# Kernel tuning notes

Measured on AMD Instinct MI355X. Metric: run time of the kernel, lower is better.

The kernel has to match this reference:

```python
import jax, jax.numpy as jnp
import numpy as np

H = 32        # num query heads
KVH = 8       # num kv heads
HD = 64       # head dim
G = H // KVH  # GQA group size
THETA = 10000.0


def _rope(x, pos):
    # x: [B, h, S, HD], pos: [B, S] int
    inv_freq = 1.0 / (THETA ** (jnp.arange(0, HD, 2, dtype=jnp.float32) / HD))  # [HD/2]
    freqs = pos.astype(jnp.float32)[:, :, None] * inv_freq[None, None, :]        # [B, S, HD/2]
    emb = jnp.concatenate([freqs, freqs], axis=-1)                               # [B, S, HD]
    cos = jnp.cos(emb)[:, None, :, :].astype(x.dtype)                            # [B, 1, S, HD]
    sin = jnp.sin(emb)[:, None, :, :].astype(x.dtype)
    x1, x2 = x[..., : HD // 2], x[..., HD // 2 :]
    rot = jnp.concatenate([-x2, x1], axis=-1)
    return x * cos + rot * sin


def setup_inputs() -> dict:
    key = jax.random.key(0)
    ks = jax.random.split(key, 8)
    B, S, D = 2, 2048, 2048
    s = 0.02
    hidden_states = jax.random.normal(ks[0], (B, S, D), dtype=jnp.float32)
    position_ids = jnp.broadcast_to(jnp.arange(S, dtype=jnp.int32)[None, :], (B, S))
    Wq = jax.random.normal(ks[1], (H * HD, D), dtype=jnp.float32) * s
    bq = jax.random.normal(ks[2], (H * HD,), dtype=jnp.float32) * s
    Wk = jax.random.normal(ks[3], (KVH * HD, D), dtype=jnp.float32) * s
    bk = jax.random.normal(ks[4], (KVH * HD,), dtype=jnp.float32) * s
    Wv = jax.random.normal(ks[5], (KVH * HD, D), dtype=jnp.float32) * s
    bv = jax.random.normal(ks[6], (KVH * HD,), dtype=jnp.float32) * s
    Wo = jax.random.normal(ks[7], (D, H * HD), dtype=jnp.float32) * s
    return dict(hidden_states=hidden_states, position_ids=position_ids,
                Wq=Wq, bq=bq, Wk=Wk, bk=bk, Wv=Wv, bv=bv, Wo=Wo)


def reference(hidden_states, position_ids, Wq, bq, Wk, bk, Wv, bv, Wo):
    B, S, D = hidden_states.shape
    scale = 1.0 / np.sqrt(HD)
    q = hidden_states @ Wq.T + bq  # [B, S, H*HD]
    k = hidden_states @ Wk.T + bk  # [B, S, KVH*HD]
    v = hidden_states @ Wv.T + bv
    q = q.reshape(B, S, H, HD).transpose(0, 2, 1, 3)      # [B, H, S, HD]
    k = k.reshape(B, S, KVH, HD).transpose(0, 2, 1, 3)    # [B, KVH, S, HD]
    v = v.reshape(B, S, KVH, HD).transpose(0, 2, 1, 3)
    q = _rope(q, position_ids)
    k = _rope(k, position_ids)
    # GQA: view q as [B, KVH, G, S, HD]; equivalent math to repeat_kv of k/v
    qg = q.reshape(B, KVH, G, S, HD)
    scores = jnp.einsum('bkgqd,bkld->bkgql', qg, k) * scale  # [B, KVH, G, S, S]
    # causal mask (past_seq_len = 0)
    causal = jnp.tril(jnp.ones((S, S), dtype=bool))
    scores = jnp.where(causal[None, None, None, :, :], scores, jnp.float32(-jnp.inf))
    attn = jax.nn.softmax(scores.astype(jnp.float32), axis=-1).astype(q.dtype)
    out = jnp.einsum('bkgql,bkld->bkgqd', attn, v)            # [B, KVH, G, S, HD]
    out = out.reshape(B, H, S, HD).transpose(0, 2, 1, 3).reshape(B, S, H * HD)
    return out @ Wo.T
```

## Files before the change

### kernel.cpp

```cpp
#include <hip/hip_runtime.h>
#include <hip/hip_bf16.h>

typedef unsigned short u16;
typedef __bf16 bf16x8 __attribute__((ext_vector_type(8)));
typedef float f32x4 __attribute__((ext_vector_type(4)));
typedef float f32x16 __attribute__((ext_vector_type(16)));
typedef float f32x4v __attribute__((ext_vector_type(4)));
typedef unsigned short u16x4 __attribute__((ext_vector_type(4)));
typedef unsigned int u32x4 __attribute__((ext_vector_type(4)));

__device__ __forceinline__ u16 f2bf(float f) {
  __bf16 h = (__bf16)f;
  return __builtin_bit_cast(unsigned short, h);
}

__device__ __forceinline__ f32x16 z16() {
  f32x16 z;
#pragma unroll
  for (int i = 0; i < 16; ++i) z[i] = 0.f;
  return z;
}

__device__ __forceinline__ int permh(int ph) {
  int blk = ph >> 4;
  int pblk = (blk == 1) ? 2 : ((blk == 2) ? 1 : blk);
  return (pblk << 4) | (ph & 15);
}

__device__ __forceinline__ int SW(int r, int c) {
  return (r << 6) + (c ^ ((r & 7) << 3));
}

#define GLOAD_LDS16(gp, lp) __builtin_amdgcn_global_load_lds( \
    (const __attribute__((address_space(1))) unsigned int*)(gp), \
    (__attribute__((address_space(3))) unsigned int*)(lp), 16, 0, 0)

#define BAR() do { asm volatile("" ::: "memory"); __builtin_amdgcn_s_barrier(); asm volatile("" ::: "memory"); } while (0)
#define VMCNT(n) asm volatile("s_waitcnt vmcnt(" #n ")" ::: "memory")
#define SBAR0() __builtin_amdgcn_sched_barrier(0)

__global__ void prep_all(const f32x4v* __restrict__ hs, u16x4* __restrict__ hsb,
                         const f32x4v* __restrict__ wq, const f32x4v* __restrict__ wk,
                         const f32x4v* __restrict__ wv, u16x4* __restrict__ wqkvb,
                         const f32x4v* __restrict__ wo, u16x4* __restrict__ wob,
                         const int* __restrict__ pos, float* __restrict__ cosT,
                         float* __restrict__ sinT, const float* __restrict__ bq,
                         const float* __restrict__ bk, const float* __restrict__ bv,
                         float* __restrict__ bc) {
  int i = blockIdx.x * 256 + threadIdx.x;
  if (i < 2097152) {
    f32x4v v = hs[i];
    u16x4 o; o.x = f2bf(v.x); o.y = f2bf(v.y); o.z = f2bf(v.z); o.w = f2bf(v.w);
    hsb[i] = o;
  } else if (i < 3670016) {
    int j = i - 2097152;
    int row = j >> 9, c4 = j & 511;
    f32x4v v;
    if (row < 2048) {
      int sr = (row & ~63) | permh(row & 63);
      v = wq[(size_t)sr * 512 + c4];
    } else if (row < 2560) {
      int rk = row - 2048;
      int sr = (rk & ~63) | permh(rk & 63);
      v = wk[(size_t)sr * 512 + c4];
    } else {
      v = wv[(size_t)(row - 2560) * 512 + c4];
    }
    u16x4 o; o.x = f2bf(v.x); o.y = f2bf(v.y); o.z = f2bf(v.z); o.w = f2bf(v.w);
    wqkvb[j] = o;
  } else if (i < 4718592) {
    int j = i - 3670016;
    f32x4v v = wo[j];
    u16x4 o; o.x = f2bf(v.x); o.y = f2bf(v.y); o.z = f2bf(v.z); o.w = f2bf(v.w);
    wob[j] = o;
  } else if (i < 4849664) {
    int j = i - 4718592;
    int bs = j >> 5, f = j & 31;
    float inv = exp2f(-(float)f * (13.287712379549449f / 32.f));
    float ang = (float)pos[bs] * inv;
    cosT[j] = cosf(ang);
    sinT[j] = sinf(ang);
  } else if (i < 4852736) {
    int j = i - 4849664;
    float v;
    if (j < 2048) {
      v = bq[(j & ~63) | permh(j & 63)];
    } else if (j < 2560) {
      int jk = j - 2048;
      v = bk[(jk & ~63) | permh(jk & 63)];
    } else {
      v = bv[j - 2560];
    }
    bc[j] = v;
  }
}

#define STAGE_A(kt, hh) { \
    const u16* s_ = aS + (size_t)(hh) * (BM / 2) * K + (size_t)(kt) * 64; \
    u16* d_ = lds + ((kt) & 1) * BUF + (hh) * (BM * 32) + wid * 512; \
    GLOAD_LDS16(s_, d_); \
    if constexpr (BM == 256) GLOAD_LDS16(s_ + (size_t)64 * K, d_ + 4096); \
  }

#define STAGE_B(kt, hh) { \
    const u16* s_ = bS + (size_t)(hh) * 128 * K + (size_t)(kt) * 64; \
    u16* d_ = lds + ((kt) & 1) * BUF + BM * 64 + (hh) * 8192 + wid * 512; \
    GLOAD_LDS16(s_, d_); \
    GLOAD_LDS16(s_ + (size_t)64 * K, d_ + 4096); \
  }

#define LDA8(buf, qm) { \
    const u16* p_ = lds + (buf) * BUF + ((qm) * (BM / 2) + arow) * 64; \
    _Pragma("unroll") \
    for (int mf = 0; mf < MF; ++mf) { \
      af[mf][0] = *(const bf16x8*)(p_ + mf * 1024 + koff0); \
      af[mf][1] = *(const bf16x8*)(p_ + mf * 1024 + koff1); \
    } }

#define LDB8(buf, qn) { \
    const u16* p_ = lds + (buf) * BUF + BM * 64 + ((qn) * 128 + brow) * 64; \
    _Pragma("unroll") \
    for (int nf = 0; nf < 2; ++nf) { \
      bfr[nf][0] = *(const bf16x8*)(p_ + nf * 1024 + koff0); \
      bfr[nf][1] = *(const bf16x8*)(p_ + nf * 1024 + koff1); \
    } }

#define MM8(qm, qn) { \
    __builtin_amdgcn_s_setprio(1); \
    _Pragma("unroll") \
    for (int mf = 0; mf < MF; ++mf) \
      _Pragma("unroll") \
      for (int nf = 0; nf < 2; ++nf) { \
        acc[(qm) * MF + mf][(qn) * 2 + nf] = __builtin_amdgcn_mfma_f32_16x16x32_bf16( \
            af[mf][0], bfr[nf][0], acc[(qm) * MF + mf][(qn) * 2 + nf], 0, 0, 0); \
        acc[(qm) * MF + mf][(qn) * 2 + nf] = __builtin_amdgcn_mfma_f32_16x16x32_bf16( \
            af[mf][1], bfr[nf][1], acc[(qm) * MF + mf][(qn) * 2 + nf], 0, 0, 0); \
      } \
    __builtin_amdgcn_s_setprio(0); }

#define VMCNT_GATE() do { if constexpr (BM == 256) { VMCNT(6); } else { VMCNT(4); } } while (0)

template <int MODE, int BM>
__global__ __launch_bounds__(512, 2) void gemm8(
    const u16* __restrict__ A, const u16* __restrict__ Bw, const int K, const int N,
    u16* __restrict__ qb, u16* __restrict__ kb, u16* __restrict__ vtb,
    const float* __restrict__ biasc, const float* __restrict__ cosT,
    const float* __restrict__ sinT, float* __restrict__ outf) {
  constexpr int MF = BM / 64;
  constexpr int BUF = BM * 64 + 16384;
  __shared__ u16 lds[2 * BUF];
  const int tid = threadIdx.x;
  const int lane = tid & 63, wid = tid >> 6;
  const int wr = wid >> 2, wc = wid & 3;
  const int col = lane & 15, rg = lane >> 4;
  const int tm = blockIdx.x, tn = blockIdx.y;

  const int srow = tid >> 3;
  const int scol = ((tid & 7) ^ (srow & 7)) * 8;
  const u16* aS = A + ((size_t)tm * BM + srow) * K + scol;
  const u16* bS = Bw + ((size_t)tn * 256 + srow) * K + scol;

  const int koff0 = (rg ^ (col & 7)) * 8;
  const int koff1 = ((4 + rg) ^ (col & 7)) * 8;
  const int arow = wr * (BM / 4) + col;
  const int brow = wc * 32 + col;

  f32x4 acc[2 * MF][4];
#pragma unroll
  for (int i = 0; i < 2 * MF; ++i)
#pragma unroll
    for (int j = 0; j < 4; ++j) acc[i][j] = (f32x4){0.f, 0.f, 0.f, 0.f};
  bf16x8 af[MF][2], bfr[2][2];

  const int ITERS = K >> 7;

  STAGE_A(0, 0); STAGE_A(0, 1);
  STAGE_B(0, 0); STAGE_B(0, 1);
  STAGE_A(1, 0); STAGE_B(1, 1); STAGE_A(1, 1);
  VMCNT_GATE();
  BAR();

#pragma unroll 1
  for (int it = 0; it < ITERS; ++it) {
    const int t0 = it * 2;
    const bool more = (it + 1 < ITERS);
    LDA8(0, 0); LDB8(0, 0);
    STAGE_B(t0 + 1, 0);
    MM8(0, 0); SBAR0(); BAR();
    LDB8(0, 1);
    if (more) STAGE_A(t0 + 2, 0);
    MM8(0, 1); SBAR0(); BAR();
    LDA8(0, 1);
    if (more) STAGE_B(t0 + 2, 1);
    MM8(1, 1); SBAR0(); BAR();
    LDB8(0, 0);
    if (more) STAGE_A(t0 + 2, 1);
    MM8(1, 0); SBAR0();
    if (more) { VMCNT_GATE(); } else { VMCNT(0); }
    BAR();
    LDA8(1, 0); LDB8(1, 0);
    if (more) STAGE_B(t0 + 2, 0);
    MM8(0, 0); SBAR0(); BAR();
    LDB8(1, 1);
    if (more) STAGE_A(t0 + 3, 0);
    MM8(0, 1); SBAR0(); BAR();
    LDA8(1, 1);
    if (more) STAGE_B(t0 + 3, 1);
    MM8(1, 1); SBAR0(); BAR();
    LDB8(1, 0);
    if (more) STAGE_A(t0 + 3, 1);
    MM8(1, 0); SBAR0();
    if (more) VMCNT_GATE();
    BAR();
  }

  if constexpr (MODE == 1) {
#pragma unroll
    for (int qm = 0; qm < 2; ++qm)
#pragma unroll
      for (int mf = 0; mf < MF; ++mf) {
        const int mbase = tm * BM + qm * (BM / 2) + wr * (BM / 4) + mf * 16 + rg * 4;
#pragma unroll
        for (int qn = 0; qn < 2; ++qn)
#pragma unroll
          for (int nf = 0; nf < 2; ++nf) {
            const int n = tn * 256 + qn * 128 + wc * 32 + nf * 16 + col;
#pragma unroll
            for (int r = 0; r < 4; ++r)
              outf[(size_t)(mbase + r) * N + n] = acc[qm * MF + mf][qn * 2 + nf][r];
          }
      }
  } else {
    if (tn < 8) {
      const float QS = 0.18033688011112042f;
#pragma unroll
      for (int qm = 0; qm < 2; ++qm)
#pragma unroll
        for (int qn = 0; qn < 2; ++qn) {
          const int h = tn * 4 + qn * 2 + (wc >> 1);
          const int c32 = wc & 1;
          const int n0 = tn * 256 + qn * 128 + wc * 32 + col;
          const float b1 = biasc[n0], b2 = biasc[n0 + 16];
          const int f = c32 * 16 + col;
          const int ph0 = c32 * 32 + col;
#pragma unroll
          for (int mf = 0; mf < MF; ++mf)
#pragma unroll
            for (int r = 0; r < 4; ++r) {
              const int m = tm * 256 + qm * 128 + wr * 64 + mf * 16 + rg * 4 + r;
              const int b = m >> 11, s = m & 2047;
              const size_t base = ((size_t)(b * 32 + h) * 2048 + s) * 64;
              float x1 = acc[qm * MF + mf][qn * 2 + 0][r] + b1;
              float x2 = acc[qm * MF + mf][qn * 2 + 1][r] + b2;
              float c = cosT[m * 32 + f], sn = sinT[m * 32 + f];
              qb[base + ph0]      = f2bf((x1 * c - x2 * sn) * QS);
              qb[base + ph0 + 16] = f2bf((x2 * c + x1 * sn) * QS);
            }
        }
    } else if (tn < 10) {
#pragma unroll
      for (int qm = 0; qm < 2; ++qm)
#pragma unroll
        for (int qn = 0; qn < 2; ++qn) {
          const int hk = (tn - 8) * 4 + qn * 2 + (wc >> 1);
          const int c32 = wc & 1;
          const int n0 = tn * 256 + qn * 128 + wc * 32 + col;
          const float b1 = biasc[n0], b2 = biasc[n0 + 16];
          const int f = c32 * 16 + col;
          const int ph0 = c32 * 32 + col;
#pragma unroll
          for (int mf = 0; mf < MF; ++mf)
#pragma unroll
            for (int r = 0; r < 4; ++r) {
              const int m = tm * 256 + qm * 128 + wr * 64 + mf * 16 + rg * 4 + r;
              const int b = m >> 11, s = m & 2047;
              const size_t base = ((size_t)(b * 8 + hk) * 2048 + s) * 64;
              float x1 = acc[qm * MF + mf][qn * 2 + 0][r] + b1;
              float x2 = acc[qm * MF + mf][qn * 2 + 1][r] + b2;
              float c = cosT[m * 32 + f], sn = sinT[m * 32 + f];
              kb[base + ph0]      = f2bf(x1 * c - x2 * sn);
              kb[base + ph0 + 16] = f2bf(x2 * c + x1 * sn);
            }
        }
    } else {
#pragma unroll
      for (int qm = 0; qm < 2; ++qm)
#pragma unroll
        for (int qn = 0; qn < 2; ++qn)
#pragma unroll
          for (int nf = 0; nf < 2; ++nf) {
            const int n = tn * 256 + qn * 128 + wc * 32 + nf * 16 + col;
            const int hk = (n - 2560) >> 6;
            const int d = (n - 2560) & 63;
            const float bvv = biasc[n];
#pragma unroll
            for (int mf = 0; mf < MF; ++mf)
#pragma unroll
              for (int r = 0; r < 4; ++r) {
                const int m = tm * 256 + qm * 128 + wr * 64 + mf * 16 + rg * 4 + r;
                const int b = m >> 11, s = m & 2047;
                vtb[((size_t)(b * 8 + hk) * 64 + d) * 2048 + s] =
                    f2bf(acc[qm * MF + mf][qn * 2 + nf][r] + bvv);
              }
          }
    }
  }
}

__global__ __launch_bounds__(256, 4) void attn_k(
    const u16* __restrict__ qb, const u16* __restrict__ kb,
    const u16* __restrict__ vtb, u16* __restrict__ attb) {
  __shared__ __align__(16) u16 Kl[3][2048];
  __shared__ __align__(16) u16 Vl[3][2048];
  const int tid = threadIdx.x, lane = tid & 63, w = tid >> 6;
  const int q32 = lane & 31, hl = lane >> 5, h4 = hl * 4;

  const int bid = blockIdx.x;
  const int xcd = bid & 7, pos = bid >> 3;
  const int grp = xcd * 8 + (pos >> 4);
  const int s0 = pos & 15;
  const int strip = ((pos >> 5) & 1) ? (15 - s0) : s0;
  const int h = grp & 31, b = grp >> 5;
  const int qb0 = (15 - strip) * 128;
  const int hk = h >> 2;
  const int q0w = qb0 + w * 32;

  const u16* Qp = qb + ((size_t)(b * 32 + h) * 2048 + q0w + q32) * 64 + hl * 8;
  bf16x8 qf[4];
#pragma unroll
  for (int s = 0; s < 4; ++s) qf[s] = *(const bf16x8*)(Qp + s * 16);

  f32x16 po[2];
  po[0] = z16(); po[1] = z16();
  float l_part = 0.f;

  const u16* Kbase = kb + (size_t)(b * 8 + hk) * 2048 * 64;
  const u16* Vbase = vtb + (size_t)(b * 8 + hk) * 64 * 2048;
  const int srow = tid >> 3, c8 = (tid & 7) << 3;
  const int cs = c8 ^ ((srow & 7) << 3);
  const u16* Ksrc = Kbase + (size_t)srow * 64 + cs;
  const u16* Vsrc = Vbase + (size_t)(srow * 2 + (cs >> 5)) * 2048 + (cs & 31);
  char* Kdst0 = (char*)Kl + w * 1024;
  char* Vdst0 = (char*)Vl + w * 1024;

  const int nkv = (qb0 >> 5) + 4;
  const int rowmax = q0w + 31;

  GLOAD_LDS16(Ksrc, Kdst0);
  GLOAD_LDS16(Vsrc, Vdst0);
  GLOAD_LDS16(Ksrc + 2048, Kdst0 + 4096);
  GLOAD_LDS16(Vsrc + 32, Vdst0 + 4096);

  for (int it = 0; it < nkv; ++it) {
    const int kv0 = it * 32;
    const int buf = it % 3;
    if (it + 2 < nkv) {
      const int b2 = (it + 2) % 3;
      GLOAD_LDS16(Ksrc + (size_t)(it + 2) * 2048, Kdst0 + b2 * 4096);
      GLOAD_LDS16(Vsrc + (size_t)(it + 2) * 32, Vdst0 + b2 * 4096);
      VMCNT(4);
    } else if (it + 1 < nkv) {
      VMCNT(2);
    } else {
      VMCNT(0);
    }
    BAR();

    if (kv0 <= rowmax) {
      const u16* Kb = (const u16*)((const char*)Kl + buf * 4096);
      const u16* Vb = (const u16*)((const char*)Vl + buf * 4096);
      const bool diag = (kv0 + 32 > q0w);

      f32x16 t = z16();
#pragma unroll
      for (int s = 0; s < 4; ++s) {
        bf16x8 kf = *(const bf16x8*)&Kb[SW(q32, s * 16 + hl * 8)];
        t = __builtin_amdgcn_mfma_f32_32x32x16_bf16(kf, qf[s], t, 0, 0, 0);
      }
      if (diag) {
        const int qg = q0w + q32;
#pragma unroll
        for (int r = 0; r < 16; ++r) {
          const int kvg = kv0 + (r & 3) + 8 * (r >> 2) + h4;
          if (kvg > qg) t[r] = -1e30f;
        }
      }
#pragma unroll
      for (int r = 0; r < 16; ++r) t[r] = __builtin_amdgcn_exp2f(t[r]);
      l_part += (((t[0] + t[1]) + (t[2] + t[3])) + ((t[4] + t[5]) + (t[6] + t[7]))) +
                (((t[8] + t[9]) + (t[10] + t[11])) + ((t[12] + t[13]) + (t[14] + t[15])));

      unsigned pw0, pw1, pw2, pw3, pw4, pw5, pw6, pw7;
      asm("v_cvt_pk_bf16_f32 %0, %1, %2" : "=v"(pw0) : "v"(t[0]), "v"(t[1]));
      asm("v_cvt_pk_bf16_f32 %0, %1, %2" : "=v"(pw1) : "v"(t[2]), "v"(t[3]));
      asm("v_cvt_pk_bf16_f32 %0, %1, %2" : "=v"(pw2) : "v"(t[4]), "v"(t[5]));
      asm("v_cvt_pk_bf16_f32 %0, %1, %2" : "=v"(pw3) : "v"(t[6]), "v"(t[7]));
      asm("v_cvt_pk_bf16_f32 %0, %1, %2" : "=v"(pw4) : "v"(t[8]), "v"(t[9]));
      asm("v_cvt_pk_bf16_f32 %0, %1, %2" : "=v"(pw5) : "v"(t[10]), "v"(t[11]));
      asm("v_cvt_pk_bf16_f32 %0, %1, %2" : "=v"(pw6) : "v"(t[12]), "v"(t[13]));
      asm("v_cvt_pk_bf16_f32 %0, %1, %2" : "=v"(pw7) : "v"(t[14]), "v"(t[15]));
      asm("v_permlane32_swap_b32 %0, %1" : "+v"(pw0), "+v"(pw2));
      asm("v_permlane32_swap_b32 %0, %1" : "+v"(pw1), "+v"(pw3));
      asm("v_permlane32_swap_b32 %0, %1" : "+v"(pw4), "+v"(pw6));
      asm("v_permlane32_swap_b32 %0, %1" : "+v"(pw5), "+v"(pw7));
      const bf16x8 pa0 = __builtin_bit_cast(bf16x8, (u32x4){pw0, pw1, pw2, pw3});
      const bf16x8 pa1 = __builtin_bit_cast(bf16x8, (u32x4){pw4, pw5, pw6, pw7});

      __builtin_amdgcn_s_setprio(1);
#pragma unroll
      for (int dblk = 0; dblk < 2; ++dblk) {
        const int d = dblk * 32 + q32;
        const int vr = d >> 1, vc = (d & 1) * 32 + hl * 8;
        bf16x8 v0 = *(const bf16x8*)&Vb[SW(vr, vc)];
        bf16x8 v1 = *(const bf16x8*)&Vb[SW(vr, vc + 16)];
        po[dblk] = __builtin_amdgcn_mfma_f32_32x32x16_bf16(pa0, v0, po[dblk], 0, 0, 0);
        po[dblk] = __builtin_amdgcn_mfma_f32_32x32x16_bf16(pa1, v1, po[dblk], 0, 0, 0);
      }
      __builtin_amdgcn_s_setprio(0);
    }
    SBAR0();
    BAR();
  }

  const float l_full = l_part + __shfl_xor(l_part, 32);
#pragma unroll
  for (int r = 0; r < 16; ++r) {
    const int qrl = (r & 3) + 8 * (r >> 2) + h4;
    const float lq = __shfl(l_full, qrl);
    const float inv = 1.f / lq;
    const size_t base = ((size_t)b * 2048 + q0w + qrl) * 2048 + h * 64;
    attb[base + q32]      = f2bf(po[0][r] * inv);
    attb[base + 32 + q32] = f2bf(po[1][r] * inv);
  }
}

extern "C" void kernel_launch(void* const* d_in, const int* in_sizes, int n_in,
                              void* d_out, int out_size, void* d_ws, size_t ws_size,
                              hipStream_t stream) {
  const float* hs = (const float*)d_in[0];
  const int* pos = (const int*)d_in[1];
  const float* Wq = (const float*)d_in[2];
  const float* bq = (const float*)d_in[3];
  const float* Wk = (const float*)d_in[4];
  const float* bk = (const float*)d_in[5];
  const float* Wv = (const float*)d_in[6];
  const float* bv = (const float*)d_in[7];
  const float* Wo = (const float*)d_in[8];
  float* out = (float*)d_out;

  char* ws = (char*)d_ws;
  size_t off = 0;
  u16* hsb = (u16*)(ws + off);   off += (size_t)4096 * 2048 * 2;
  u16* wqkvb = (u16*)(ws + off); off += (size_t)3072 * 2048 * 2;
  u16* wob = (u16*)(ws + off);   off += (size_t)2048 * 2048 * 2;
  float* biasc = (float*)(ws + off); off += 3072 * 4;
  float* cosT = (float*)(ws + off);  off += (size_t)4096 * 32 * 4;
  float* sinT = (float*)(ws + off);  off += (size_t)4096 * 32 * 4;
  u16* qb = (u16*)(ws + off);    off += (size_t)2 * 32 * 2048 * 64 * 2;
  u16* kb = (u16*)(ws + off);    off += (size_t)2 * 8 * 2048 * 64 * 2;
  u16* vtb = (u16*)(ws + off);   off += (size_t)2 * 8 * 64 * 2048 * 2;
  u16* attb = (u16*)(ws + off);  off += (size_t)4096 * 2048 * 2;

  prep_all<<<18956, 256, 0, stream>>>((const f32x4v*)hs, (u16x4*)hsb,
                                      (const f32x4v*)Wq, (const f32x4v*)Wk,
                                      (const f32x4v*)Wv, (u16x4*)wqkvb,
                                      (const f32x4v*)Wo, (u16x4*)wob,
                                      pos, cosT, sinT, bq, bk, bv, biasc);

  gemm8<0, 256><<<dim3(16, 12), 512, 0, stream>>>(hsb, wqkvb, 2048, 3072,
                                                  qb, kb, vtb, biasc, cosT, sinT, nullptr);
  attn_k<<<1024, 256, 0, stream>>>(qb, kb, vtb, attb);
  gemm8<1, 128><<<dim3(32, 8), 512, 0, stream>>>(attb, wob, 2048, 2048,
                                                 nullptr, nullptr, nullptr, nullptr,
                                                 nullptr, nullptr, out);
}
```

Measured before the change: 172.5 us.

## Rewrite projection GEMMs with register double-buffered fragments and new tile shapes

Replaces the 8-phase quadrant-based GEMM with a new kernel that double-buffers A/B fragments in registers (aX/aY, bA/bB), loading the next k-slice's fragments while the current MFMAs run. The warp layout changes to 4x2, with 256-row M tiles and a configurable BN: 192 for the QKV projection (16x16 grid, 256 blocks) and 128 for the output projection. The epilogue is reworked to route Q, K and V columns per fragment pair, since a 192-wide tile can span regions. The intent is better CU occupancy (256 blocks instead of 192 for QKV) and overlap of LDS reads with MFMA, at the cost of more waitcnt and barrier synchronisation per iteration.

Result: slower. 219.9 us (+27.4%).

```diff
diff --git a/kernel.cpp b/kernel.cpp
--- a/kernel.cpp
+++ b/kernel.cpp
@@ -37,6 +37,7 @@
 
 #define BAR() do { asm volatile("" ::: "memory"); __builtin_amdgcn_s_barrier(); asm volatile("" ::: "memory"); } while (0)
 #define VMCNT(n) asm volatile("s_waitcnt vmcnt(" #n ")" ::: "memory")
+#define LG0() asm volatile("s_waitcnt lgkmcnt(0)" ::: "memory")
 #define SBAR0() __builtin_amdgcn_sched_barrier(0)
 
 __global__ void prep_all(const f32x4v* __restrict__ hs, u16x4* __restrict__ hsb,
@@ -95,214 +96,174 @@
   }
 }
 
-#define STAGE_A(kt, hh) { \
-    const u16* s_ = aS + (size_t)(hh) * (BM / 2) * K + (size_t)(kt) * 64; \
-    u16* d_ = lds + ((kt) & 1) * BUF + (hh) * (BM * 32) + wid * 512; \
-    GLOAD_LDS16(s_, d_); \
-    if constexpr (BM == 256) GLOAD_LDS16(s_ + (size_t)64 * K, d_ + 4096); \
-  }
-
-#define STAGE_B(kt, hh) { \
-    const u16* s_ = bS + (size_t)(hh) * 128 * K + (size_t)(kt) * 64; \
-    u16* d_ = lds + ((kt) & 1) * BUF + BM * 64 + (hh) * 8192 + wid * 512; \
-    GLOAD_LDS16(s_, d_); \
-    GLOAD_LDS16(s_ + (size_t)64 * K, d_ + 4096); \
-  }
-
-#define LDA8(buf, qm) { \
-    const u16* p_ = lds + (buf) * BUF + ((qm) * (BM / 2) + arow) * 64; \
+#define RSTAGE_A(kt, c) GLOAD_LDS16( \
+    aS + (size_t)((c) * 64) * K + (size_t)(kt) * 64, \
+    lds + ((kt) & 1) * BUFSZ + (c) * 4096 + tid * 8)
+
+#define RSTAGE_B(kt, c) GLOAD_LDS16( \
+    bS + (size_t)((c) * 64) * K + (size_t)(kt) * 64, \
+    lds + ((kt) & 1) * BUFSZ + 16384 + (c) * 4096 + tid * 8)
+
+#define STAGE_H1(kt) { RSTAGE_A(kt, 0); RSTAGE_A(kt, 1); RSTAGE_A(kt, 2); \
+    if constexpr (NB == 3) RSTAGE_A(kt, 3); }
+#define STAGE_H2(kt) { if constexpr (NB == 2) RSTAGE_A(kt, 3); \
+    RSTAGE_B(kt, 0); RSTAGE_B(kt, 1); if constexpr (NB == 3) RSTAGE_B(kt, 2); }
+
+#define RLDA(dst, buf, kof) { \
+    const u16* p_ = lds + (buf) * BUFSZ + arow * 64; \
     _Pragma("unroll") \
-    for (int mf = 0; mf < MF; ++mf) { \
-      af[mf][0] = *(const bf16x8*)(p_ + mf * 1024 + koff0); \
-      af[mf][1] = *(const bf16x8*)(p_ + mf * 1024 + koff1); \
-    } }
-
-#define LDB8(buf, qn) { \
-    const u16* p_ = lds + (buf) * BUF + BM * 64 + ((qn) * 128 + brow) * 64; \
+    for (int mf = 0; mf < 4; ++mf) dst[mf] = *(const bf16x8*)(p_ + mf * 1024 + (kof)); }
+
+#define RLDB(dst, buf, kof) { \
+    const u16* p_ = lds + (buf) * BUFSZ + 16384 + brow * 64; \
     _Pragma("unroll") \
-    for (int nf = 0; nf < 2; ++nf) { \
-      bfr[nf][0] = *(const bf16x8*)(p_ + nf * 1024 + koff0); \
-      bfr[nf][1] = *(const bf16x8*)(p_ + nf * 1024 + koff1); \
-    } }
-
-#define MM8(qm, qn) { \
+    for (int nf = 0; nf < NF; ++nf) dst[nf] = *(const bf16x8*)(p_ + nf * 1024 + (kof)); }
+
+#define RMM(afs, bfs) { \
     __builtin_amdgcn_s_setprio(1); \
     _Pragma("unroll") \
-    for (int mf = 0; mf < MF; ++mf) \
+    for (int mf = 0; mf < 4; ++mf) \
       _Pragma("unroll") \
-      for (int nf = 0; nf < 2; ++nf) { \
-        acc[(qm) * MF + mf][(qn) * 2 + nf] = __builtin_amdgcn_mfma_f32_16x16x32_bf16( \
-            af[mf][0], bfr[nf][0], acc[(qm) * MF + mf][(qn) * 2 + nf], 0, 0, 0); \
-        acc[(qm) * MF + mf][(qn) * 2 + nf] = __builtin_amdgcn_mfma_f32_16x16x32_bf16( \
-            af[mf][1], bfr[nf][1], acc[(qm) * MF + mf][(qn) * 2 + nf], 0, 0, 0); \
-      } \
+      for (int nf = 0; nf < NF; ++nf) \
+        acc[mf][nf] = __builtin_amdgcn_mfma_f32_16x16x32_bf16(afs[mf], bfs[nf], acc[mf][nf], 0, 0, 0); \
     __builtin_amdgcn_s_setprio(0); }
 
-#define VMCNT_GATE() do { if constexpr (BM == 256) { VMCNT(6); } else { VMCNT(4); } } while (0)
-
-template <int MODE, int BM>
-__global__ __launch_bounds__(512, 2) void gemm8(
+template <int MODE, int BN>
+__global__ __launch_bounds__(512, 2) void gemm_ra(
     const u16* __restrict__ A, const u16* __restrict__ Bw, const int K, const int N,
     u16* __restrict__ qb, u16* __restrict__ kb, u16* __restrict__ vtb,
     const float* __restrict__ biasc, const float* __restrict__ cosT,
     const float* __restrict__ sinT, float* __restrict__ outf) {
-  constexpr int MF = BM / 64;
-  constexpr int BUF = BM * 64 + 16384;
-  __shared__ u16 lds[2 * BUF];
+  constexpr int NF = BN / 32;
+  constexpr int NB = BN / 64;
+  constexpr int BUFSZ = (256 + BN) * 64;
+  __shared__ u16 lds[2 * BUFSZ];
   const int tid = threadIdx.x;
   const int lane = tid & 63, wid = tid >> 6;
-  const int wr = wid >> 2, wc = wid & 3;
+  const int wr = wid >> 1, wc = wid & 1;
   const int col = lane & 15, rg = lane >> 4;
   const int tm = blockIdx.x, tn = blockIdx.y;
 
   const int srow = tid >> 3;
   const int scol = ((tid & 7) ^ (srow & 7)) * 8;
-  const u16* aS = A + ((size_t)tm * BM + srow) * K + scol;
-  const u16* bS = Bw + ((size_t)tn * 256 + srow) * K + scol;
+  const u16* aS = A + ((size_t)tm * 256 + srow) * K + scol;
+  const u16* bS = Bw + ((size_t)tn * BN + srow) * K + scol;
 
   const int koff0 = (rg ^ (col & 7)) * 8;
   const int koff1 = ((4 + rg) ^ (col & 7)) * 8;
-  const int arow = wr * (BM / 4) + col;
-  const int brow = wc * 32 + col;
-
-  f32x4 acc[2 * MF][4];
-#pragma unroll
-  for (int i = 0; i < 2 * MF; ++i)
-#pragma unroll
-    for (int j = 0; j < 4; ++j) acc[i][j] = (f32x4){0.f, 0.f, 0.f, 0.f};
-  bf16x8 af[MF][2], bfr[2][2];
+  const int arow = wr * 64 + col;
+  const int brow = wc * (BN / 2) + col;
+
+  f32x4 acc[4][NF];
+#pragma unroll
+  for (int i = 0; i < 4; ++i)
+#pragma unroll
+    for (int j = 0; j < NF; ++j) acc[i][j] = (f32x4){0.f, 0.f, 0.f, 0.f};
+  bf16x8 aX[4], aY[4], bA[NF], bB[NF];
 
   const int ITERS = K >> 7;
 
-  STAGE_A(0, 0); STAGE_A(0, 1);
-  STAGE_B(0, 0); STAGE_B(0, 1);
-  STAGE_A(1, 0); STAGE_B(1, 1); STAGE_A(1, 1);
-  VMCNT_GATE();
+  STAGE_H1(0); STAGE_H2(0); STAGE_H1(1); STAGE_H2(1);
+  if constexpr (NB == 3) { VMCNT(7); } else { VMCNT(6); }
   BAR();
+  RLDA(aX, 0, koff0); RLDB(bA, 0, koff0);
 
 #pragma unroll 1
   for (int it = 0; it < ITERS; ++it) {
-    const int t0 = it * 2;
     const bool more = (it + 1 < ITERS);
-    LDA8(0, 0); LDB8(0, 0);
-    STAGE_B(t0 + 1, 0);
-    MM8(0, 0); SBAR0(); BAR();
-    LDB8(0, 1);
-    if (more) STAGE_A(t0 + 2, 0);
-    MM8(0, 1); SBAR0(); BAR();
-    LDA8(0, 1);
-    if (more) STAGE_B(t0 + 2, 1);
-    MM8(1, 1); SBAR0(); BAR();
-    LDB8(0, 0);
-    if (more) STAGE_A(t0 + 2, 1);
-    MM8(1, 0); SBAR0();
-    if (more) { VMCNT_GATE(); } else { VMCNT(0); }
+    if (it > 0) STAGE_H2(2 * it + 1);
+    RLDA(aY, 0, koff1); RLDB(bB, 0, koff1);
+    RMM(aX, bA);
+    LG0(); VMCNT(0); BAR();
+    if (more) STAGE_H1(2 * it + 2);
+    RLDA(aX, 1, koff0); RLDB(bA, 1, koff0);
+    RMM(aY, bB);
+    LG0(); BAR();
+    if (more) STAGE_H2(2 * it + 2);
+    RLDA(aY, 1, koff1); RLDB(bB, 1, koff1);
+    RMM(aX, bA);
+    LG0();
+    if (more) VMCNT(0);
     BAR();
-    LDA8(1, 0); LDB8(1, 0);
-    if (more) STAGE_B(t0 + 2, 0);
-    MM8(0, 0); SBAR0(); BAR();
-    LDB8(1, 1);
-    if (more) STAGE_A(t0 + 3, 0);
-    MM8(0, 1); SBAR0(); BAR();
-    LDA8(1, 1);
-    if (more) STAGE_B(t0 + 3, 1);
-    MM8(1, 1); SBAR0(); BAR();
-    LDB8(1, 0);
-    if (more) STAGE_A(t0 + 3, 1);
-    MM8(1, 0); SBAR0();
-    if (more) VMCNT_GATE();
-    BAR();
+    if (more) {
+      STAGE_H1(2 * it + 3);
+      RLDA(aX, 0, koff0); RLDB(bA, 0, koff0);
+    }
+    RMM(aY, bB);
+    LG0(); BAR();
   }
 
   if constexpr (MODE == 1) {
 #pragma unroll
-    for (int qm = 0; qm < 2; ++qm)
-#pragma unroll
-      for (int mf = 0; mf < MF; ++mf) {
-        const int mbase = tm * BM + qm * (BM / 2) + wr * (BM / 4) + mf * 16 + rg * 4;
-#pragma unroll
-        for (int qn = 0; qn < 2; ++qn)
-#pragma unroll
-          for (int nf = 0; nf < 2; ++nf) {
-            const int n = tn * 256 + qn * 128 + wc * 32 + nf * 16 + col;
-#pragma unroll
-            for (int r = 0; r < 4; ++r)
-              outf[(size_t)(mbase + r) * N + n] = acc[qm * MF + mf][qn * 2 + nf][r];
+    for (int mf = 0; mf < 4; ++mf) {
+      const int mbase = tm * 256 + wr * 64 + mf * 16 + rg * 4;
+#pragma unroll
+      for (int nf = 0; nf < NF; ++nf) {
+        const int n = tn * BN + wc * (BN / 2) + nf * 16 + col;
+#pragma unroll
+        for (int r = 0; r < 4; ++r)
+          outf[(size_t)(mbase + r) * N + n] = acc[mf][nf][r];
+      }
+    }
+  } else {
+    const float QS = 0.18033688011112042f;
+#pragma unroll
+    for (int nf = 0; nf < NF; nf += 2) {
+      const int n0p = tn * BN + wc * (BN / 2) + nf * 16;
+      if (n0p < 2048) {
+        const int h = n0p >> 6;
+        const int c32 = (n0p >> 5) & 1;
+        const float b1 = biasc[n0p + col], b2 = biasc[n0p + 16 + col];
+        const int f = c32 * 16 + col, ph0 = c32 * 32 + col;
+#pragma unroll
+        for (int mf = 0; mf < 4; ++mf)
+#pragma unroll
+          for (int r = 0; r < 4; ++r) {
+            const int m = tm * 256 + wr * 64 + mf * 16 + rg * 4 + r;
+            const int b = m >> 11, s = m & 2047;
+            const size_t base = ((size_t)(b * 32 + h) * 2048 + s) * 64;
+            float x1 = acc[mf][nf][r] + b1;
+            float x2 = acc[mf][nf + 1][r] + b2;
+            float c = cosT[m * 32 + f], sn = sinT[m * 32 + f];
+            qb[base + ph0]      = f2bf((x1 * c - x2 * sn) * QS);
+            qb[base + ph0 + 16] = f2bf((x2 * c + x1 * sn) * QS);
           }
-      }
-  } else {
-    if (tn < 8) {
-      const float QS = 0.18033688011112042f;
-#pragma unroll
-      for (int qm = 0; qm < 2; ++qm)
-#pragma unroll
-        for (int qn = 0; qn < 2; ++qn) {
-          const int h = tn * 4 + qn * 2 + (wc >> 1);
-          const int c32 = wc & 1;
-          const int n0 = tn * 256 + qn * 128 + wc * 32 + col;
-          const float b1 = biasc[n0], b2 = biasc[n0 + 16];
-          const int f = c32 * 16 + col;
-          const int ph0 = c32 * 32 + col;
-#pragma unroll
-          for (int mf = 0; mf < MF; ++mf)
+      } else if (n0p < 2560) {
+        const int hk = (n0p - 2048) >> 6;
+        const int c32 = (n0p >> 5) & 1;
+        const float b1 = biasc[n0p + col], b2 = biasc[n0p + 16 + col];
+        const int f = c32 * 16 + col, ph0 = c32 * 32 + col;
+#pragma unroll
+        for (int mf = 0; mf < 4; ++mf)
+#pragma unroll
+          for (int r = 0; r < 4; ++r) {
+            const int m = tm * 256 + wr * 64 + mf * 16 + rg * 4 + r;
+            const int b = m >> 11, s = m & 2047;
+            const size_t base = ((size_t)(b * 8 + hk) * 2048 + s) * 64;
+            float x1 = acc[mf][nf][r] + b1;
+            float x2 = acc[mf][nf + 1][r] + b2;
+            float c = cosT[m * 32 + f], sn = sinT[m * 32 + f];
+            kb[base + ph0]      = f2bf(x1 * c - x2 * sn);
+            kb[base + ph0 + 16] = f2bf(x2 * c + x1 * sn);
+          }
+      } else {
+#pragma unroll
+        for (int dd = 0; dd < 2; ++dd) {
+          const int nn = n0p + dd * 16;
+          const int hv = (nn - 2560) >> 6;
+          const int dbase = ((nn - 2560) & 63) + col;
+          const float bvv = biasc[nn + col];
+#pragma unroll
+          for (int mf = 0; mf < 4; ++mf)
 #pragma unroll
             for (int r = 0; r < 4; ++r) {
-              const int m = tm * 256 + qm * 128 + wr * 64 + mf * 16 + rg * 4 + r;
+              const int m = tm * 256 + wr * 64 + mf * 16 + rg * 4 + r;
               const int b = m >> 11, s = m & 2047;
-              const size_t base = ((size_t)(b * 32 + h) * 2048 + s) * 64;
-              float x1 = acc[qm * MF + mf][qn * 2 + 0][r] + b1;
-              float x2 = acc[qm * MF + mf][qn * 2 + 1][r] + b2;
-              float c = cosT[m * 32 + f], sn = sinT[m * 32 + f];
-              qb[base + ph0]      = f2bf((x1 * c - x2 * sn) * QS);
-              qb[base + ph0 + 16] = f2bf((x2 * c + x1 * sn) * QS);
+              vtb[((size_t)(b * 8 + hv) * 64 + dbase) * 2048 + s] =
+                  f2bf(acc[mf][nf + dd][r] + bvv);
             }
         }
-    } else if (tn < 10) {
-#pragma unroll
-      for (int qm = 0; qm < 2; ++qm)
-#pragma unroll
-        for (int qn = 0; qn < 2; ++qn) {
-          const int hk = (tn - 8) * 4 + qn * 2 + (wc >> 1);
-          const int c32 = wc & 1;
-          const int n0 = tn * 256 + qn * 128 + wc * 32 + col;
-          const float b1 = biasc[n0], b2 = biasc[n0 + 16];
-          const int f = c32 * 16 + col;
-          const int ph0 = c32 * 32 + col;
-#pragma unroll
-          for (int mf = 0; mf < MF; ++mf)
-#pragma unroll
-            for (int r = 0; r < 4; ++r) {
-              const int m = tm * 256 + qm * 128 + wr * 64 + mf * 16 + rg * 4 + r;
-              const int b = m >> 11, s = m & 2047;
-              const size_t base = ((size_t)(b * 8 + hk) * 2048 + s) * 64;
-              float x1 = acc[qm * MF + mf][qn * 2 + 0][r] + b1;
-              float x2 = acc[qm * MF + mf][qn * 2 + 1][r] + b2;
-              float c = cosT[m * 32 + f], sn = sinT[m * 32 + f];
-              kb[base + ph0]      = f2bf(x1 * c - x2 * sn);
-              kb[base + ph0 + 16] = f2bf(x2 * c + x1 * sn);
-            }
-        }
-    } else {
-#pragma unroll
-      for (int qm = 0; qm < 2; ++qm)
-#pragma unroll
-        for (int qn = 0; qn < 2; ++qn)
-#pragma unroll
-          for (int nf = 0; nf < 2; ++nf) {
-            const int n = tn * 256 + qn * 128 + wc * 32 + nf * 16 + col;
-            const int hk = (n - 2560) >> 6;
-            const int d = (n - 2560) & 63;
-            const float bvv = biasc[n];
-#pragma unroll
-            for (int mf = 0; mf < MF; ++mf)
-#pragma unroll
-              for (int r = 0; r < 4; ++r) {
-                const int m = tm * 256 + qm * 128 + wr * 64 + mf * 16 + rg * 4 + r;
-                const int b = m >> 11, s = m & 2047;
-                vtb[((size_t)(b * 8 + hk) * 64 + d) * 2048 + s] =
-                    f2bf(acc[qm * MF + mf][qn * 2 + nf][r] + bvv);
-              }
-          }
+      }
     }
   }
 }
@@ -467,10 +428,10 @@
                                       (const f32x4v*)Wo, (u16x4*)wob,
                                       pos, cosT, sinT, bq, bk, bv, biasc);
 
-  gemm8<0, 256><<<dim3(16, 12), 512, 0, stream>>>(hsb, wqkvb, 2048, 3072,
-                                                  qb, kb, vtb, biasc, cosT, sinT, nullptr);
+  gemm_ra<0, 192><<<dim3(16, 16), 512, 0, stream>>>(hsb, wqkvb, 2048, 3072,
+                                                    qb, kb, vtb, biasc, cosT, sinT, nullptr);
   attn_k<<<1024, 256, 0, stream>>>(qb, kb, vtb, attb);
-  gemm8<1, 128><<<dim3(32, 8), 512, 0, stream>>>(attb, wob, 2048, 2048,
-                                                 nullptr, nullptr, nullptr, nullptr,
-                                                 nullptr, nullptr, out);
-}
+  gemm_ra<1, 128><<<dim3(16, 16), 512, 0, stream>>>(attb, wob, 2048, 2048,
+                                                    nullptr, nullptr, nullptr, nullptr,
+                                                    nullptr, nullptr, out);
+}
```

## Replace output projection GEMM with dedicated double-buffered 256x128 tile kernel

Applied to the files above, without the earlier changes.

Adds a specialized gemm_o kernel for the output projection. It uses 256x128 tiles staged into LDS with direct global-to-LDS loads in half-tile stages, and double-buffered register fragments so LDS reads overlap MFMA work. It raises wave priority around the MFMA blocks. It replaces the generic gemm8 launch (previously 32x8 blocks) with a 16x16 grid, aiming at better latency hiding and occupancy control for this GEMM. The risks are the hand-tuned waitcnt and barrier schedule, and fewer blocks per CU.

New measurement: 172.2 us, median of 2. No clear change (-0.2%).

```diff
diff --git a/kernel.cpp b/kernel.cpp
--- a/kernel.cpp
+++ b/kernel.cpp
@@ -37,6 +37,7 @@
 
 #define BAR() do { asm volatile("" ::: "memory"); __builtin_amdgcn_s_barrier(); asm volatile("" ::: "memory"); } while (0)
 #define VMCNT(n) asm volatile("s_waitcnt vmcnt(" #n ")" ::: "memory")
+#define LG0() asm volatile("s_waitcnt lgkmcnt(0)" ::: "memory")
 #define SBAR0() __builtin_amdgcn_sched_barrier(0)
 
 __global__ void prep_all(const f32x4v* __restrict__ hs, u16x4* __restrict__ hsb,
@@ -307,6 +308,110 @@
   }
 }
 
+#define RSTAGE_A(kt, c) GLOAD_LDS16( \
+    aS + (size_t)((c) * 64) * K + (size_t)(kt) * 64, \
+    lds + ((kt) & 1) * BUFSZ + (c) * 4096 + tid * 8)
+
+#define RSTAGE_B(kt, c) GLOAD_LDS16( \
+    bS + (size_t)((c) * 64) * K + (size_t)(kt) * 64, \
+    lds + ((kt) & 1) * BUFSZ + 16384 + (c) * 4096 + tid * 8)
+
+#define STAGE_H1(kt) { RSTAGE_A(kt, 0); RSTAGE_A(kt, 1); RSTAGE_A(kt, 2); }
+#define STAGE_H2(kt) { RSTAGE_A(kt, 3); RSTAGE_B(kt, 0); RSTAGE_B(kt, 1); }
+
+#define RLDA(dst, buf, kof) { \
+    const u16* p_ = lds + (buf) * BUFSZ + arow * 64; \
+    _Pragma("unroll") \
+    for (int mf = 0; mf < 4; ++mf) dst[mf] = *(const bf16x8*)(p_ + mf * 1024 + (kof)); }
+
+#define RLDB(dst, buf, kof) { \
+    const u16* p_ = lds + (buf) * BUFSZ + 16384 + brow * 64; \
+    _Pragma("unroll") \
+    for (int nf = 0; nf < 4; ++nf) dst[nf] = *(const bf16x8*)(p_ + nf * 1024 + (kof)); }
+
+#define RMM(afs, bfs) { \
+    __builtin_amdgcn_s_setprio(1); \
+    _Pragma("unroll") \
+    for (int mf = 0; mf < 4; ++mf) \
+      _Pragma("unroll") \
+      for (int nf = 0; nf < 4; ++nf) \
+        acc[mf][nf] = __builtin_amdgcn_mfma_f32_16x16x32_bf16(afs[mf], bfs[nf], acc[mf][nf], 0, 0, 0); \
+    __builtin_amdgcn_s_setprio(0); }
+
+__global__ void __launch_bounds__(512)
+__attribute__((amdgpu_waves_per_eu(2, 2)))
+gemm_o(const u16* __restrict__ A, const u16* __restrict__ Bw, const int K, const int N,
+       float* __restrict__ outf) {
+  constexpr int BUFSZ = (256 + 128) * 64;
+  __shared__ u16 lds[2 * BUFSZ];
+  const int tid = threadIdx.x;
+  const int lane = tid & 63, wid = tid >> 6;
+  const int wr = wid >> 1, wc = wid & 1;
+  const int col = lane & 15, rg = lane >> 4;
+  const int tm = blockIdx.x, tn = blockIdx.y;
+
+  const int srow = tid >> 3;
+  const int scol = ((tid & 7) ^ (srow & 7)) * 8;
+  const u16* aS = A + ((size_t)tm * 256 + srow) * K + scol;
+  const u16* bS = Bw + ((size_t)tn * 128 + srow) * K + scol;
+
+  const int koff0 = (rg ^ (col & 7)) * 8;
+  const int koff1 = ((4 + rg) ^ (col & 7)) * 8;
+  const int arow = wr * 64 + col;
+  const int brow = wc * 64 + col;
+
+  f32x4 acc[4][4];
+#pragma unroll
+  for (int i = 0; i < 4; ++i)
+#pragma unroll
+    for (int j = 0; j < 4; ++j) acc[i][j] = (f32x4){0.f, 0.f, 0.f, 0.f};
+  bf16x8 aX[4], aY[4], bA[4], bB[4];
+
+  const int ITERS = K >> 7;
+
+  STAGE_H1(0); STAGE_H2(0); STAGE_H1(1); STAGE_H2(1);
+  VMCNT(6);
+  BAR();
+  RLDA(aX, 0, koff0); RLDB(bA, 0, koff0);
+
+#pragma unroll 1
+  for (int it = 0; it < ITERS; ++it) {
+    const bool more = (it + 1 < ITERS);
+    if (it > 0) STAGE_H2(2 * it + 1);
+    RLDA(aY, 0, koff1); RLDB(bB, 0, koff1);
+    RMM(aX, bA);
+    LG0(); VMCNT(0); BAR();
+    if (more) STAGE_H1(2 * it + 2);
+    RLDA(aX, 1, koff0); RLDB(bA, 1, koff0);
+    RMM(aY, bB);
+    LG0(); BAR();
+    if (more) STAGE_H2(2 * it + 2);
+    RLDA(aY, 1, koff1); RLDB(bB, 1, koff1);
+    RMM(aX, bA);
+    LG0();
+    if (more) VMCNT(0);
+    BAR();
+    if (more) {
+      STAGE_H1(2 * it + 3);
+      RLDA(aX, 0, koff0); RLDB(bA, 0, koff0);
+    }
+    RMM(aY, bB);
+    LG0(); BAR();
+  }
+
+#pragma unroll
+  for (int mf = 0; mf < 4; ++mf) {
+    const int mbase = tm * 256 + wr * 64 + mf * 16 + rg * 4;
+#pragma unroll
+    for (int nf = 0; nf < 4; ++nf) {
+      const int n = tn * 128 + wc * 64 + nf * 16 + col;
+#pragma unroll
+      for (int r = 0; r < 4; ++r)
+        outf[(size_t)(mbase + r) * N + n] = acc[mf][nf][r];
+    }
+  }
+}
+
 __global__ __launch_bounds__(256, 4) void attn_k(
     const u16* __restrict__ qb, const u16* __restrict__ kb,
     const u16* __restrict__ vtb, u16* __restrict__ attb) {
@@ -470,7 +575,5 @@
   gemm8<0, 256><<<dim3(16, 12), 512, 0, stream>>>(hsb, wqkvb, 2048, 3072,
                                                   qb, kb, vtb, biasc, cosT, sinT, nullptr);
   attn_k<<<1024, 256, 0, stream>>>(qb, kb, vtb, attb);
-  gemm8<1, 128><<<dim3(32, 8), 512, 0, stream>>>(attb, wob, 2048, 2048,
-                                                 nullptr, nullptr, nullptr, nullptr,
-                                                 nullptr, nullptr, out);
-}
+  gemm_o<<<dim3(16, 16), 512, 0, stream>>>(attb, wob, 2048, 2048, out);
+}
```
